# Kernel optimization log

Measured on AMD Instinct MI355X. Metric: run time of the kernel, lower is better.

The kernel has to match this reference:

```python
import jax, jax.numpy as jnp
import numpy as np

N = 8192        # points
M = 131072      # query-key pairs (edges)
C_IN = 512
H = 8           # heads
D = 64          # head_channels
BINS = 48
BIN_SIZE = 0.05


def setup_inputs() -> dict:
    key = jax.random.key(0)
    ks = jax.random.split(key, 8)
    x_F = jax.random.normal(ks[0], (N, C_IN), dtype=jnp.float32)
    x_C = jax.random.uniform(ks[1], (N, 3), dtype=jnp.float32)
    qk_pair_idxs = jax.random.randint(ks[2], (2, M), 0, N, dtype=jnp.int64)
    W_qkv = jax.random.normal(ks[3], (C_IN, 3 * H * D), dtype=jnp.float32) * 0.02
    b_qkv = jnp.zeros((3 * H * D,), dtype=jnp.float32)
    q_tables = jax.random.normal(ks[4], (3, BINS, H, D), dtype=jnp.float32) * 0.02
    k_tables = jax.random.normal(ks[5], (3, BINS, H, D), dtype=jnp.float32) * 0.02
    v_tables = jax.random.normal(ks[6], (3, BINS, H, D), dtype=jnp.float32) * 0.02
    return {"x_F": x_F, "x_C": x_C, "qk_pair_idxs": qk_pair_idxs,
            "W_qkv": W_qkv, "b_qkv": b_qkv,
            "q_tables": q_tables, "k_tables": k_tables, "v_tables": v_tables}


def reference(x_F, x_C, qk_pair_idxs, W_qkv, b_qkv, q_tables, k_tables, v_tables):
    n = x_F.shape[0]
    qkv = (x_F @ W_qkv + b_qkv).reshape(n, 3, H, D)
    q = qkv[:, 0] * (D ** -0.5)   # scale folded into queries, as in the module
    k = qkv[:, 1]
    v = qkv[:, 2]
    qi = qk_pair_idxs[0]
    ki = qk_pair_idxs[1]
    # quantized relative coordinates -> table bin indices [M,3]
    rel = (x_C[qi] - x_C[ki]) / BIN_SIZE + BINS / 2
    idx = jnp.clip(rel.astype(jnp.int32), 0, BINS - 1)
    # precompute per-point, per-axis, per-bin table dot products [N,3,BINS,H]
    q_dot = jnp.einsum('nhd,abhd->nabh', q, q_tables)
    k_dot = jnp.einsum('nhd,abhd->nabh', k, k_tables)
    # content logits [M,H]
    logits = jnp.einsum('mhd,mhd->mh', q[qi], k[ki])
    for a in range(3):  # fixed xyz axes
        logits = logits + q_dot[qi, a, idx[:, a]] + k_dot[ki, a, idx[:, a]]
    # scatter softmax over query index (per head)
    seg_max = jax.ops.segment_max(logits, qi, num_segments=n)
    e = jnp.exp(logits - seg_max[qi])
    denom = jax.ops.segment_sum(e, qi, num_segments=n)
    attn = e / denom[qi]  # [M,H]
    # value-side relative position bias, summed over axes [M,H,D]
    vt = v_tables[0, idx[:, 0]] + v_tables[1, idx[:, 1]] + v_tables[2, idx[:, 2]]
    contrib = attn[:, :, None] * (v[ki] + vt)            # [M,H,D]
    agg = jax.ops.segment_sum(contrib, qi, num_segments=n)  # [N,H,D]
    return agg.reshape(n, H * D)
```

## Files before the change

### kernel.cpp

```cpp
#include <hip/hip_runtime.h>
#include <hip/hip_bf16.h>
#include <stdint.h>

#define N_PTS 8192
#define M_EDGES 131072
#define CIN 512
#define QKV_COLS 1536

typedef __bf16 bf16x8 __attribute__((ext_vector_type(8)));
typedef float f32x4 __attribute__((ext_vector_type(4)));

#define GAS __attribute__((address_space(1)))
#define LAS __attribute__((address_space(3)))

__device__ __forceinline__ void gload_lds16(const void* g, void* l) {
  __builtin_amdgcn_global_load_lds((const GAS void*)g, (LAS void*)l, 16, 0, 0);
}

__global__ __launch_bounds__(256) void prep_kernel(
    const float* __restrict__ xF, const float* __restrict__ W,
    const float* __restrict__ qt, const float* __restrict__ kt,
    const float* __restrict__ vt, const int* __restrict__ pairs,
    const float* __restrict__ xc,
    __bf16* __restrict__ A, __bf16* __restrict__ BT,
    __bf16* __restrict__ qtb, __bf16* __restrict__ ktb, __bf16* __restrict__ vtT,
    int* __restrict__ qi_a, unsigned* __restrict__ pack0, int* __restrict__ cnt) {
  __shared__ float tile[32][33];
  int b = blockIdx.x;
  int tid = threadIdx.x;
  if (b < 4096) {
    int base = (b * 256 + tid) * 4;
    float4 v = *(const float4*)(xF + base);
    A[base + 0] = (__bf16)v.x;
    A[base + 1] = (__bf16)v.y;
    A[base + 2] = (__bf16)v.z;
    A[base + 3] = (__bf16)v.w;
  } else if (b < 4864) {
    int blk = b - 4096;
    int bk = blk & 15, bn = blk >> 4;
    int x = tid & 31, y = tid >> 5;
#pragma unroll
    for (int j = 0; j < 4; j++) {
      int r = y + j * 8;
      tile[r][x] = W[(size_t)(bk * 32 + r) * QKV_COLS + bn * 32 + x];
    }
    __syncthreads();
#pragma unroll
    for (int j = 0; j < 4; j++) {
      int r = y + j * 8;
      BT[(size_t)(bn * 32 + r) * CIN + bk * 32 + x] = (__bf16)tile[x][r];
    }
  } else if (b < 5152) {
    int i = (b - 4864) * 256 + tid;
    int d = i & 63, h = (i >> 6) & 7, ab = i >> 9;
    int po = (h * 144 + ab) * 64 + d;
    qtb[po] = (__bf16)qt[i];
    ktb[po] = (__bf16)kt[i];
  } else if (b < 5472) {
    int i = (b - 5152) * 256 + tid;
    int p = i % 160;
    int d = (i / 160) & 63;
    int h = i / 10240;
    vtT[i] = (p < 144) ? (__bf16)vt[p * 512 + h * 64 + d] : (__bf16)0.f;
  } else {
    int m = (b - 5472) * 256 + tid;
    int qi = pairs[m], ki = pairs[M_EDGES + m];
    unsigned pb = 0;
#pragma unroll
    for (int a = 0; a < 3; a++) {
      float rel = (xc[qi * 3 + a] - xc[ki * 3 + a]) / 0.05f + 24.0f;
      int bb = (int)rel;
      bb = bb < 0 ? 0 : (bb > 47 ? 47 : bb);
      pb |= (unsigned)bb << (6 * a);
    }
    qi_a[m] = qi;
    pack0[m] = (unsigned)ki | (pb << 13);
    atomicAdd(&cnt[qi], 1);
  }
}

__global__ __launch_bounds__(256) void gemm_scan_kernel(
    const __bf16* __restrict__ A, const __bf16* __restrict__ BT,
    const float* __restrict__ bias, __bf16* __restrict__ qb,
    __bf16* __restrict__ kv,
    const int* __restrict__ cnt, int* __restrict__ off, int* __restrict__ cursor) {
  __shared__ __align__(16) char At[2][64 * 128];
  __shared__ __align__(16) char Bt[2][128 * 128];
  __shared__ int wsum[4];
  int bid = blockIdx.x;
  int tid = threadIdx.x;

  if (bid == 1536) {
    int lane = tid & 63, w = tid >> 6;
    int local[32];
    int s = 0;
#pragma unroll
    for (int i = 0; i < 8; i++) {
      int4 v = ((const int4*)cnt)[tid * 8 + i];
      local[i * 4 + 0] = v.x; local[i * 4 + 1] = v.y;
      local[i * 4 + 2] = v.z; local[i * 4 + 3] = v.w;
      s += v.x + v.y + v.z + v.w;
    }
    int incl = s;
#pragma unroll
    for (int d = 1; d < 64; d <<= 1) {
      int t = __shfl_up(incl, d, 64);
      if (lane >= d) incl += t;
    }
    if (lane == 63) wsum[w] = incl;
    __syncthreads();
    int woff = 0;
#pragma unroll
    for (int j = 0; j < 4; j++) woff += (j < w) ? wsum[j] : 0;
    int run = woff + incl - s;
    int base = tid * 32;
#pragma unroll
    for (int i = 0; i < 32; i++) {
      off[base + i] = run;
      cursor[base + i] = run;
      run += local[i];
    }
    if (tid == 255) off[N_PTS] = run;
    return;
  }

  int bn = bid % 12, bm = bid / 12;
  int w = tid >> 6, l = tid & 63;
  int wm = w & 1, wn = w >> 1;
  f32x4 acc[2][4] = {};
  const char* Ab = (const char*)A;
  const char* Bb = (const char*)BT;
  int lr = l & 15;
  int lk = (l >> 4) * 16;
  int xr = (lr & 7) << 4;

  auto stage = [&](int tk, int buf) {
#pragma unroll
    for (int r = 0; r < 2; r++) {
      int flat = r * 4096 + tid * 16;
      int row = flat >> 7, colb = flat & 127;
      int gcolb = colb ^ ((row & 7) << 4);
      gload_lds16(Ab + ((size_t)(bm * 64 + row) * CIN + tk * 64) * 2 + gcolb,
                  At[buf] + r * 4096 + w * 1024);
    }
#pragma unroll
    for (int r = 0; r < 4; r++) {
      int flat = r * 4096 + tid * 16;
      int row = flat >> 7, colb = flat & 127;
      int gcolb = colb ^ ((row & 7) << 4);
      gload_lds16(Bb + ((size_t)(bn * 128 + row) * CIN + tk * 64) * 2 + gcolb,
                  Bt[buf] + r * 4096 + w * 1024);
    }
  };

  stage(0, 0);
  __syncthreads();
  int cur = 0;
  for (int kt = 0; kt < 8; kt++) {
    if (kt < 7) stage(kt + 1, cur ^ 1);
#pragma unroll
    for (int ks = 0; ks < 2; ks++) {
      bf16x8 af[2], bfr[4];
      int cs = (ks * 64 + lk) ^ xr;
#pragma unroll
      for (int mf = 0; mf < 2; mf++) af[mf] = *(const bf16x8*)(At[cur] + (wm * 32 + mf * 16 + lr) * 128 + cs);
#pragma unroll
      for (int nf = 0; nf < 4; nf++) bfr[nf] = *(const bf16x8*)(Bt[cur] + (wn * 64 + nf * 16 + lr) * 128 + cs);
#pragma unroll
      for (int mf = 0; mf < 2; mf++)
#pragma unroll
        for (int nf = 0; nf < 4; nf++)
          acc[mf][nf] = __builtin_amdgcn_mfma_f32_16x16x32_bf16(af[mf], bfr[nf], acc[mf][nf], 0, 0, 0);
    }
    __syncthreads();
    cur ^= 1;
  }

  int lg = l >> 4;
#pragma unroll
  for (int mf = 0; mf < 2; mf++) {
#pragma unroll
    for (int nf = 0; nf < 4; nf++) {
      int gc = bn * 128 + wn * 64 + nf * 16 + lr;
      float b = bias[gc];
      int which = gc >> 9;
      int col = gc & 511;
      float scale = which == 0 ? 0.125f : 1.0f;
#pragma unroll
      for (int j = 0; j < 4; j++) {
        int gr = bm * 64 + wm * 32 + mf * 16 + lg * 4 + j;
        float val = (acc[mf][nf][j] + b) * scale;
        if (which == 0) qb[(size_t)gr * 512 + col] = (__bf16)val;
        else kv[(size_t)gr * 1024 + (which == 2 ? 512 : 0) + col] = (__bf16)val;
      }
    }
  }
}

__global__ __launch_bounds__(256) void td_scatter_kernel(
    const __bf16* __restrict__ qb, const __bf16* __restrict__ kv,
    const __bf16* __restrict__ qtb, const __bf16* __restrict__ ktb,
    __bf16* __restrict__ qdot, __bf16* __restrict__ kdot,
    const int* __restrict__ qi_a, const unsigned* __restrict__ pack0,
    int* __restrict__ cursor, unsigned* __restrict__ epack) {
  __shared__ __align__(16) char As[128 * 128];
  __shared__ __align__(16) char Bs[144 * 128];
  int bid = blockIdx.x;
  int tid = threadIdx.x;

  if (bid < 512) {
    int m = bid * 256 + tid;
    int qi = qi_a[m];
    int pos = atomicAdd(&cursor[qi], 1);
    epack[pos] = pack0[m];
    return;
  }

  int td = bid - 512;
  int nt = td & 63, h = (td >> 6) & 7, z = td >> 9;
  const __bf16* src = z ? kv : qb;
  const __bf16* tab = z ? ktb : qtb;
  __bf16* out = z ? kdot : qdot;
  size_t SB = z ? 2048 : 1024;
  int w = tid >> 6, l = tid & 63;
  const char* sb = (const char*)src;
  const char* tb = (const char*)tab + (size_t)h * 144 * 128;
#pragma unroll
  for (int p = 0; p < 4; p++) {
    int flat = p * 4096 + tid * 16;
    int row = flat >> 7, colb = flat & 127;
    int gcolb = colb ^ ((row & 7) << 4);
    gload_lds16(sb + (size_t)(nt * 128 + row) * SB + h * 128 + gcolb, As + p * 4096 + w * 1024);
    gload_lds16(tb + row * 128 + gcolb, Bs + p * 4096 + w * 1024);
  }
  if (w < 2) {
    int flat = 16384 + w * 1024 + l * 16;
    int row = flat >> 7, colb = flat & 127;
    int gcolb = colb ^ ((row & 7) << 4);
    gload_lds16(tb + row * 128 + gcolb, Bs + 16384 + w * 1024);
  }
  __syncthreads();

  f32x4 acc[2][9] = {};
  int lr = l & 15, lk = (l >> 4) * 16;
  int xr = (lr & 7) << 4;
#pragma unroll
  for (int ks = 0; ks < 2; ks++) {
    bf16x8 af[2], bf[9];
    int cs = (ks * 64 + lk) ^ xr;
#pragma unroll
    for (int mf = 0; mf < 2; mf++)
      af[mf] = *(const bf16x8*)(As + (w * 32 + mf * 16 + lr) * 128 + cs);
#pragma unroll
    for (int nf = 0; nf < 9; nf++)
      bf[nf] = *(const bf16x8*)(Bs + (nf * 16 + lr) * 128 + cs);
#pragma unroll
    for (int mf = 0; mf < 2; mf++)
#pragma unroll
      for (int nf = 0; nf < 9; nf++)
        acc[mf][nf] = __builtin_amdgcn_mfma_f32_16x16x32_bf16(af[mf], bf[nf], acc[mf][nf], 0, 0, 0);
  }

  int lg = l >> 4;
#pragma unroll
  for (int mf = 0; mf < 2; mf++)
#pragma unroll
    for (int nf = 0; nf < 9; nf++)
#pragma unroll
      for (int j = 0; j < 4; j++) {
        int n = nt * 128 + w * 32 + mf * 16 + lg * 4 + j;
        int ab = nf * 16 + lr;
        out[(size_t)n * 1152 + ab * 8 + h] = (__bf16)acc[mf][nf][j];
      }
}

__global__ __launch_bounds__(256) void attn_kernel(
    const __bf16* __restrict__ qb, const __bf16* __restrict__ kv,
    const __bf16* __restrict__ qdot, const __bf16* __restrict__ kdot,
    const int* __restrict__ off, const unsigned* __restrict__ epack,
    float* __restrict__ num, float* __restrict__ den, __bf16* __restrict__ Hb) {
  __shared__ float hist[8 * 164];
  __shared__ float part[4][512];
  __shared__ float dpart[4][8];
  int n = blockIdx.x;
  int tid = threadIdx.x;
  int w = tid >> 6, l = tid & 63;
  int h = l >> 3, dg = l & 7;

  for (int i = tid; i < 8 * 164; i += 256) hist[i] = 0.f;
  __syncthreads();

  bf16x8 q8 = *(const bf16x8*)(qb + (n << 9) + l * 8);
  float qv[8];
#pragma unroll
  for (int j = 0; j < 8; j++) qv[j] = (float)q8[j];

  float acc[8] = {0.f, 0.f, 0.f, 0.f, 0.f, 0.f, 0.f, 0.f};
  float dn = 0.f;
  int e0 = off[n], e1 = off[n + 1];
  const __bf16* qd_row = qdot + (size_t)n * 1152;
  int axis = dg < 3 ? dg : dg - 3;
  int tsh = 6 * axis;

  for (int e = e0 + w; e < e1; e += 4) {
    unsigned pk = epack[__builtin_amdgcn_readfirstlane(e)];
    int ki = pk & 8191;
    unsigned pb = pk >> 13;
    bf16x8 k8 = *(const bf16x8*)(kv + ((size_t)ki << 10) + l * 8);
    bf16x8 v8 = *(const bf16x8*)(kv + ((size_t)ki << 10) + 512 + l * 8);
    int bin = (int)((pb >> tsh) & 63u);
    int idx = (axis * 48 + bin) * 8 + h;
    const __bf16* tbl = dg < 3 ? qd_row : (kdot + (size_t)ki * 1152);
    float p = (dg < 6) ? (float)tbl[idx] : 0.f;
#pragma unroll
    for (int j = 0; j < 8; j++) p += qv[j] * (float)k8[j];
    p += __shfl_xor(p, 1, 64);
    p += __shfl_xor(p, 2, 64);
    p += __shfl_xor(p, 4, 64);
    float x = __expf(p);
    dn += x;
#pragma unroll
    for (int j = 0; j < 8; j++) acc[j] += x * (float)v8[j];
    if (dg == 0) {
      float* hh = hist + h * 164;
      atomicAdd(hh + (pb & 63), x);
      atomicAdd(hh + 48 + ((pb >> 6) & 63), x);
      atomicAdd(hh + 96 + ((pb >> 12) & 63), x);
    }
  }

  f32x4 a0 = {acc[0], acc[1], acc[2], acc[3]};
  f32x4 a1 = {acc[4], acc[5], acc[6], acc[7]};
  *(f32x4*)&part[w][l * 8] = a0;
  *(f32x4*)&part[w][l * 8 + 4] = a1;
  if (dg == 0) dpart[w][h] = dn;
  __syncthreads();

#pragma unroll
  for (int half = 0; half < 2; half++) {
    int idx = tid + half * 256;
    float s = 0.f;
#pragma unroll
    for (int ww = 0; ww < 4; ww++) s += part[ww][idx];
    num[(n << 9) + idx] = s;
  }
  if (tid < 8) {
    float d = 0.f;
#pragma unroll
    for (int ww = 0; ww < 4; ww++) d += dpart[ww][tid];
    den[n * 8 + tid] = d;
  }
  for (int i = tid; i < 1280; i += 256) {
    int hh = i / 160, p = i % 160;
    Hb[(size_t)n * 1280 + i] = (__bf16)hist[hh * 164 + p];
  }
}

__global__ __launch_bounds__(256) void finish_kernel(const __bf16* __restrict__ Hb,
                                                     const __bf16* __restrict__ vtT,
                                                     const float* __restrict__ den,
                                                     float* __restrict__ out) {
  __shared__ __align__(16) char As[2][128 * 64];
  __shared__ __align__(16) char Bs[2][64 * 64];
  int nt = blockIdx.x, h = blockIdx.y;
  int tid = threadIdx.x, w = tid >> 6, l = tid & 63;
  int lr = l & 15, lk = (l >> 4) * 16;
  int xr = (lr & 3) << 4;
  const char* Ab = (const char*)Hb;
  const char* Bb = (const char*)vtT;
  f32x4 acc[2][4] = {};

  auto stage = [&](int tk, int buf) {
#pragma unroll
    for (int c = 0; c < 2; c++) {
      int flat = c * 4096 + tid * 16;
      int row = flat >> 6, colb = flat & 63;
      int gcolb = colb ^ ((row & 3) << 4);
      gload_lds16(Ab + ((size_t)(nt * 128 + row) * 1280 + h * 160 + tk * 32) * 2 + gcolb,
                  As[buf] + c * 4096 + w * 1024);
    }
    {
      int flat = tid * 16;
      int row = flat >> 6, colb = flat & 63;
      int gcolb = colb ^ ((row & 3) << 4);
      gload_lds16(Bb + ((size_t)(h * 64 + row) * 160 + tk * 32) * 2 + gcolb,
                  Bs[buf] + w * 1024);
    }
  };

  stage(0, 0);
  __syncthreads();
  int cur = 0;
  for (int kt = 0; kt < 5; kt++) {
    if (kt < 4) stage(kt + 1, cur ^ 1);
    bf16x8 af[2], bf[4];
    int cs = lk ^ xr;
#pragma unroll
    for (int mf = 0; mf < 2; mf++) af[mf] = *(const bf16x8*)(As[cur] + (w * 32 + mf * 16 + lr) * 64 + cs);
#pragma unroll
    for (int nf = 0; nf < 4; nf++) bf[nf] = *(const bf16x8*)(Bs[cur] + (nf * 16 + lr) * 64 + cs);
#pragma unroll
    for (int mf = 0; mf < 2; mf++)
#pragma unroll
      for (int nf = 0; nf < 4; nf++)
        acc[mf][nf] = __builtin_amdgcn_mfma_f32_16x16x32_bf16(af[mf], bf[nf], acc[mf][nf], 0, 0, 0);
    __syncthreads();
    cur ^= 1;
  }

  int lg = l >> 4;
#pragma unroll
  for (int mf = 0; mf < 2; mf++) {
#pragma unroll
    for (int j = 0; j < 4; j++) {
      int n = nt * 128 + w * 32 + mf * 16 + lg * 4 + j;
      float dnv = den[n * 8 + h];
      float inv = dnv > 0.f ? 1.f / dnv : 0.f;
#pragma unroll
      for (int nf = 0; nf < 4; nf++) {
        int gi = (n << 9) + h * 64 + nf * 16 + lr;
        out[gi] = (out[gi] + acc[mf][nf][j]) * inv;
      }
    }
  }
}

extern "C" void kernel_launch(void* const* d_in, const int* in_sizes, int n_in,
                              void* d_out, int out_size, void* d_ws, size_t ws_size,
                              hipStream_t stream) {
  const float* xF = (const float*)d_in[0];
  const float* xC = (const float*)d_in[1];
  const int* pairs = (const int*)d_in[2];
  const float* W = (const float*)d_in[3];
  const float* bias = (const float*)d_in[4];
  const float* qt = (const float*)d_in[5];
  const float* kt = (const float*)d_in[6];
  const float* vt = (const float*)d_in[7];
  float* out = (float*)d_out;

  char* ws = (char*)d_ws;
  size_t o = 0;
  auto alloc = [&](size_t bytes) {
    void* p = ws + o;
    o = (o + bytes + 255) & ~(size_t)255;
    return p;
  };
  char* region0 = (char*)alloc((size_t)N_PTS * 1280 * 2);
  __bf16* A = (__bf16*)region0;
  __bf16* BT = (__bf16*)(region0 + (size_t)N_PTS * CIN * 2);
  __bf16* Hb = (__bf16*)region0;
  __bf16* qb = (__bf16*)alloc((size_t)N_PTS * 512 * 2);
  __bf16* kv = (__bf16*)alloc((size_t)N_PTS * 1024 * 2);
  __bf16* qtb = (__bf16*)alloc((size_t)8 * 144 * 64 * 2);
  __bf16* ktb = (__bf16*)alloc((size_t)8 * 144 * 64 * 2);
  __bf16* vtT = (__bf16*)alloc((size_t)8 * 64 * 160 * 2);
  __bf16* qdot = (__bf16*)alloc((size_t)N_PTS * 1152 * 2);
  __bf16* kdot = (__bf16*)alloc((size_t)N_PTS * 1152 * 2);
  float* den = (float*)alloc((size_t)N_PTS * 8 * 4);
  int* qi_a = (int*)alloc(M_EDGES * 4);
  unsigned* pack0 = (unsigned*)alloc(M_EDGES * 4);
  unsigned* epack = (unsigned*)alloc(M_EDGES * 4);
  int* cnt = (int*)alloc(N_PTS * 4);
  int* off = (int*)alloc((N_PTS + 1) * 4);
  int* cursor = (int*)alloc(N_PTS * 4);

  hipMemsetAsync(cnt, 0, N_PTS * 4, stream);

  prep_kernel<<<5984, 256, 0, stream>>>(xF, W, qt, kt, vt, pairs, xC,
                                        A, BT, qtb, ktb, vtT, qi_a, pack0, cnt);
  gemm_scan_kernel<<<1537, 256, 0, stream>>>(A, BT, bias, qb, kv, cnt, off, cursor);
  td_scatter_kernel<<<1536, 256, 0, stream>>>(qb, kv, qtb, ktb, qdot, kdot,
                                              qi_a, pack0, cursor, epack);
  attn_kernel<<<N_PTS, 256, 0, stream>>>(qb, kv, qdot, kdot, off, epack, out, den, Hb);
  finish_kernel<<<dim3(N_PTS / 128, 8), 256, 0, stream>>>(Hb, vtT, den, out);
}
```

Baseline: 151.4 us.

## Schedule attention blocks by descending degree, halve block size, store numerator as bf16

```diff
diff --git a/kernel.cpp b/kernel.cpp
--- a/kernel.cpp
+++ b/kernel.cpp
@@ -83,10 +83,13 @@
     const __bf16* __restrict__ A, const __bf16* __restrict__ BT,
     const float* __restrict__ bias, __bf16* __restrict__ qb,
     __bf16* __restrict__ kv,
-    const int* __restrict__ cnt, int* __restrict__ off, int* __restrict__ cursor) {
+    const int* __restrict__ cnt, int* __restrict__ off, int* __restrict__ cursor,
+    int* __restrict__ qperm) {
   __shared__ __align__(16) char At[2][64 * 128];
   __shared__ __align__(16) char Bt[2][128 * 128];
   __shared__ int wsum[4];
+  __shared__ int hist2[64];
+  __shared__ int bpos[64];
   int bid = blockIdx.x;
   int tid = threadIdx.x;
 
@@ -108,6 +111,7 @@
       if (lane >= d) incl += t;
     }
     if (lane == 63) wsum[w] = incl;
+    if (tid < 64) hist2[tid] = 0;
     __syncthreads();
     int woff = 0;
 #pragma unroll
@@ -119,8 +123,23 @@
       off[base + i] = run;
       cursor[base + i] = run;
       run += local[i];
+      int c = local[i] < 63 ? local[i] : 63;
+      atomicAdd(&hist2[c], 1);
     }
     if (tid == 255) off[N_PTS] = run;
+    __syncthreads();
+    if (tid < 64) {
+      int p = 0;
+      for (int bb = 63; bb > tid; bb--) p += hist2[bb];
+      bpos[tid] = p;
+    }
+    __syncthreads();
+#pragma unroll
+    for (int i = 0; i < 32; i++) {
+      int c = local[i] < 63 ? local[i] : 63;
+      int pos = atomicAdd(&bpos[c], 1);
+      qperm[pos] = base + i;
+    }
     return;
   }
 
@@ -274,20 +293,21 @@
       }
 }
 
-__global__ __launch_bounds__(256) void attn_kernel(
+__global__ __launch_bounds__(128) void attn_kernel(
     const __bf16* __restrict__ qb, const __bf16* __restrict__ kv,
     const __bf16* __restrict__ qdot, const __bf16* __restrict__ kdot,
     const int* __restrict__ off, const unsigned* __restrict__ epack,
-    float* __restrict__ num, float* __restrict__ den, __bf16* __restrict__ Hb) {
+    const int* __restrict__ qperm,
+    __bf16* __restrict__ numb, float* __restrict__ den, __bf16* __restrict__ Hb) {
   __shared__ float hist[8 * 164];
-  __shared__ float part[4][512];
-  __shared__ float dpart[4][8];
-  int n = blockIdx.x;
+  __shared__ float part[2][512];
+  __shared__ float dpart[2][8];
+  int n = qperm[blockIdx.x];
   int tid = threadIdx.x;
   int w = tid >> 6, l = tid & 63;
   int h = l >> 3, dg = l & 7;
 
-  for (int i = tid; i < 8 * 164; i += 256) hist[i] = 0.f;
+  for (int i = tid; i < 8 * 164; i += 128) hist[i] = 0.f;
   __syncthreads();
 
   bf16x8 q8 = *(const bf16x8*)(qb + (n << 9) + l * 8);
@@ -302,7 +322,7 @@
   int axis = dg < 3 ? dg : dg - 3;
   int tsh = 6 * axis;
 
-  for (int e = e0 + w; e < e1; e += 4) {
+  for (int e = e0 + w; e < e1; e += 2) {
     unsigned pk = epack[__builtin_amdgcn_readfirstlane(e)];
     int ki = pk & 8191;
     unsigned pb = pk >> 13;
@@ -336,21 +356,10 @@
   if (dg == 0) dpart[w][h] = dn;
   __syncthreads();
 
-#pragma unroll
-  for (int half = 0; half < 2; half++) {
-    int idx = tid + half * 256;
-    float s = 0.f;
-#pragma unroll
-    for (int ww = 0; ww < 4; ww++) s += part[ww][idx];
-    num[(n << 9) + idx] = s;
-  }
-  if (tid < 8) {
-    float d = 0.f;
-#pragma unroll
-    for (int ww = 0; ww < 4; ww++) d += dpart[ww][tid];
-    den[n * 8 + tid] = d;
-  }
-  for (int i = tid; i < 1280; i += 256) {
+  for (int idx = tid; idx < 512; idx += 128)
+    numb[(n << 9) + idx] = (__bf16)(part[0][idx] + part[1][idx]);
+  if (tid < 8) den[n * 8 + tid] = dpart[0][tid] + dpart[1][tid];
+  for (int i = tid; i < 1280; i += 128) {
     int hh = i / 160, p = i % 160;
     Hb[(size_t)n * 1280 + i] = (__bf16)hist[hh * 164 + p];
   }
@@ -358,6 +367,7 @@
 
 __global__ __launch_bounds__(256) void finish_kernel(const __bf16* __restrict__ Hb,
                                                      const __bf16* __restrict__ vtT,
+                                                     const __bf16* __restrict__ numb,
                                                      const float* __restrict__ den,
                                                      float* __restrict__ out) {
   __shared__ __align__(16) char As[2][128 * 64];
@@ -419,7 +429,7 @@
 #pragma unroll
       for (int nf = 0; nf < 4; nf++) {
         int gi = (n << 9) + h * 64 + nf * 16 + lr;
-        out[gi] = (out[gi] + acc[mf][nf][j]) * inv;
+        out[gi] = ((float)numb[gi] + acc[mf][nf][j]) * inv;
       }
     }
   }
@@ -456,6 +466,7 @@
   __bf16* vtT = (__bf16*)alloc((size_t)8 * 64 * 160 * 2);
   __bf16* qdot = (__bf16*)alloc((size_t)N_PTS * 1152 * 2);
   __bf16* kdot = (__bf16*)alloc((size_t)N_PTS * 1152 * 2);
+  __bf16* numb = (__bf16*)alloc((size_t)N_PTS * 512 * 2);
   float* den = (float*)alloc((size_t)N_PTS * 8 * 4);
   int* qi_a = (int*)alloc(M_EDGES * 4);
   unsigned* pack0 = (unsigned*)alloc(M_EDGES * 4);
@@ -463,14 +474,16 @@
   int* cnt = (int*)alloc(N_PTS * 4);
   int* off = (int*)alloc((N_PTS + 1) * 4);
   int* cursor = (int*)alloc(N_PTS * 4);
+  int* qperm = (int*)alloc(N_PTS * 4);
 
   hipMemsetAsync(cnt, 0, N_PTS * 4, stream);
 
   prep_kernel<<<5984, 256, 0, stream>>>(xF, W, qt, kt, vt, pairs, xC,
                                         A, BT, qtb, ktb, vtT, qi_a, pack0, cnt);
-  gemm_scan_kernel<<<1537, 256, 0, stream>>>(A, BT, bias, qb, kv, cnt, off, cursor);
+  gemm_scan_kernel<<<1537, 256, 0, stream>>>(A, BT, bias, qb, kv, cnt, off, cursor, qperm);
   td_scatter_kernel<<<1536, 256, 0, stream>>>(qb, kv, qtb, ktb, qdot, kdot,
                                               qi_a, pack0, cursor, epack);
-  attn_kernel<<<N_PTS, 256, 0, stream>>>(qb, kv, qdot, kdot, off, epack, out, den, Hb);
-  finish_kernel<<<dim3(N_PTS / 128, 8), 256, 0, stream>>>(Hb, vtT, den, out);
-}
+  attn_kernel<<<N_PTS, 128, 0, stream>>>(qb, kv, qdot, kdot, off, epack, qperm,
+                                         numb, den, Hb);
+  finish_kernel<<<dim3(N_PTS / 128, 8), 256, 0, stream>>>(Hb, vtT, numb, den, out);
+}
```

Result: faster. 148.1 us (-2.2%).
